# Optimization experiments

Hardware: AMD Instinct MI355X
Metric: run time of the kernel (lower is better)

Reference implementation:

```python
import jax, jax.numpy as jnp
import numpy as np

STEPS = 10      # raymarch_steps
HIDDEN = 16     # LSTM hidden size (hardcoded in module)
F_CH = 256      # num_feature_channels
B, N = 4, 8192  # batch, rays per batch element


def setup_inputs() -> dict:
    key = jax.random.key(0)
    ks = jax.random.split(key, 16)
    # rigid cam2world: random rotation (QR) + translation, bottom row [0,0,0,1]
    Q, _ = jnp.linalg.qr(jax.random.normal(ks[0], (B, 3, 3)))
    t = 0.5 * jax.random.normal(ks[1], (B, 3)) + jnp.array([0.0, 0.0, -2.5])
    cam2world = (jnp.zeros((B, 4, 4))
                 .at[:, :3, :3].set(Q)
                 .at[:, :3, 3].set(t)
                 .at[:, 3, 3].set(1.0))
    uv = jax.random.uniform(ks[2], (B, N, 2)) * 128.0  # pixel coords, 128x128 image
    intrinsics = jnp.tile(jnp.array([[128.0, 0.0, 64.0],
                                     [0.0, 128.0, 64.0],
                                     [0.0, 0.0, 1.0]]), (B, 1, 1))
    # torch forward draws N(0.05, 0.0005); lifted to an input for determinism
    initial_depth = 0.05 + 0.0005 * jax.random.normal(ks[3], (B, N, 1))
    g = lambda k, s, fan: jax.random.normal(k, s) * (1.0 / np.sqrt(fan))
    W1 = g(ks[4], (3, F_CH), 3); b1 = jnp.zeros((F_CH,))
    W2 = g(ks[5], (F_CH, F_CH), F_CH); b2 = jnp.zeros((F_CH,))
    W3 = g(ks[6], (F_CH, F_CH), F_CH); b3 = jnp.zeros((F_CH,))
    w_ih = g(ks[7], (4 * HIDDEN, F_CH), F_CH)
    w_hh = g(ks[8], (4 * HIDDEN, HIDDEN), HIDDEN)
    # forget-gate bias init = 1 (lstm_forget_gate_init fills [n//4:n//2] of each bias)
    fg = jnp.zeros((4 * HIDDEN,)).at[HIDDEN:2 * HIDDEN].set(1.0)
    b_ih = fg; b_hh = fg
    w_out = g(ks[9], (1, HIDDEN), HIDDEN); b_out = jnp.zeros((1,))
    return dict(cam2world=cam2world, uv=uv, intrinsics=intrinsics,
                initial_depth=initial_depth, W1=W1, b1=b1, W2=W2, b2=b2,
                W3=W3, b3=b3, w_ih=w_ih, w_hh=w_hh, b_ih=b_ih, b_hh=b_hh,
                w_out=w_out, b_out=b_out)


def world_from_xy_depth(xy, depth, intrinsics, cam2world):
    fx = intrinsics[:, 0:1, 0]; fy = intrinsics[:, 1:2, 1]
    cx = intrinsics[:, 0:1, 2]; cy = intrinsics[:, 1:2, 2]
    z = depth[..., 0]                                   # (B,N)
    x_lift = (xy[..., 0] - cx) / fx * z
    y_lift = (xy[..., 1] - cy) / fy * z
    pts_cam = jnp.stack([x_lift, y_lift, z, jnp.ones_like(z)], axis=-1)  # (B,N,4)
    return jnp.einsum('bij,bnj->bni', cam2world, pts_cam)[..., :3]


def get_ray_directions(xy, cam2world, intrinsics):
    z = jnp.ones(xy.shape[:2] + (1,), xy.dtype)
    pts = world_from_xy_depth(xy, z, intrinsics, cam2world)
    rd = pts - cam2world[:, None, :3, 3]
    return rd / jnp.linalg.norm(rd, axis=-1, keepdims=True)


def depth_from_world(world_coords, cam2world):
    hom = jnp.concatenate([world_coords, jnp.ones_like(world_coords[..., :1])], axis=-1)
    cam = jnp.einsum('bij,bnj->bni', jnp.linalg.inv(cam2world), hom)
    return cam[..., 2:3]


# identity in fwd, clamps grad to [-10,10] in bwd (matches register_hook in torch)
@jax.custom_vjp
def grad_clamp(x):
    return x

def _gc_fwd(x):
    return x, None

def _gc_bwd(_, g):
    return (jnp.clip(g, -10.0, 10.0),)

grad_clamp.defvjp(_gc_fwd, _gc_bwd)


def reference(cam2world, uv, intrinsics, initial_depth,
              W1, b1, W2, b2, W3, b3, w_ih, w_hh, b_ih, b_hh, w_out, b_out):
    B_, N_ = uv.shape[:2]
    ray_dirs = get_ray_directions(uv, cam2world, intrinsics)      # (B,N,3)
    wc0 = world_from_xy_depth(uv, initial_depth, intrinsics, cam2world)

    def phi(x):  # (B,N,3) -> (B,N,F_CH)
        h = jax.nn.relu(x @ W1 + b1)
        h = jax.nn.relu(h @ W2 + b2)
        return h @ W3 + b3

    def step(carry, _):
        wc, h, c = carry
        v = phi(wc).reshape(-1, F_CH)                             # (B*N, F)
        gates = v @ w_ih.T + b_ih + h @ w_hh.T + b_hh             # (B*N, 4H)
        i, f, g, o = jnp.split(gates, 4, axis=-1)
        c_new = jax.nn.sigmoid(f) * c + jax.nn.sigmoid(i) * jnp.tanh(g)
        h_new = grad_clamp(jax.nn.sigmoid(o) * jnp.tanh(c_new))
        sd = (h_new @ w_out.T + b_out).reshape(B_, N_, 1)         # signed distance
        return (wc + ray_dirs * sd, h_new, c_new), None

    h0 = jnp.zeros((B_ * N_, HIDDEN), uv.dtype)
    c0 = jnp.zeros((B_ * N_, HIDDEN), uv.dtype)
    (wc, _, _), _ = jax.lax.scan(step, (wc0, h0, c0), None, length=STEPS)
    return wc, depth_from_world(wc, cam2world)
```

## Files before the change

### kernel.cpp

```cpp
#include <hip/hip_runtime.h>
#include <hip/hip_bf16.h>


typedef __attribute__((ext_vector_type(8)))  __bf16 bf16x8;
typedef __attribute__((ext_vector_type(4)))  __bf16 bf16x4;
typedef __attribute__((ext_vector_type(4)))  float  f32x4;

#define H1S 264
#define H2S 296
#define GPAD 68

static __device__ __forceinline__ float sigmoidf_(float x) {
  return 1.0f / (1.0f + __expf(-x));
}
static __device__ __forceinline__ float tanhf_(float x) {
  return 1.0f - 2.0f / (__expf(2.0f * x) + 1.0f);
}
static __device__ __forceinline__ float ldin(const void* p, int i, bool f32) {
  return f32 ? ((const float*)p)[i] : (float)(((const __bf16*)p)[i]);
}
static __device__ __forceinline__ bool probe_f32(const void* intr) {
  return (*(const unsigned*)intr) == 0x43000000u;
}

__global__ void prep_kernel(const void* __restrict__ W2,
                            const void* __restrict__ W3,
                            const void* __restrict__ w_ih,
                            const void* __restrict__ b3,
                            const void* __restrict__ b_ih,
                            const void* __restrict__ b_hh,
                            const void* __restrict__ w_hh,
                            const void* __restrict__ intr,
                            __bf16* __restrict__ w2p,
                            __bf16* __restrict__ wfp,
                            float* __restrict__ bfv) {
  const bool f32 = probe_f32(intr);
  const int t = threadIdx.x;
  const int blk = blockIdx.x;
  __shared__ float stg[12480];

  if (blk < 256) {
    int idx = blk * 256 + t;
    int j = idx & 7, l = (idx >> 3) & 63, kt = (idx >> 9) & 7, nt = idx >> 12;
    int k = kt * 32 + ((l >> 4) << 3) + j;
    int n = nt * 16 + (l & 15);
    w2p[idx] = (__bf16)ldin(W2, k * 256 + n, f32);
  } else if (blk < 288) {
    int bb = blk - 256;
    int gt = bb >> 3, kt = bb & 7;
    float* wih_s = stg;
    float* w3_s = stg + 16 * 260;
    for (int i = t; i < 16 * 256; i += 256)
      wih_s[(i >> 8) * 260 + (i & 255)] =
          ldin(w_ih, (gt * 16 + (i >> 8)) * 256 + (i & 255), f32);
    for (int i = t; i < 32 * 256; i += 256)
      w3_s[(i >> 8) * 260 + (i & 255)] =
          ldin(W3, (kt * 32 + (i >> 8)) * 256 + (i & 255), f32);
    __syncthreads();
    #pragma unroll
    for (int h = 0; h < 2; ++h) {
      int o = t + h * 256;
      int l = o >> 3, j = o & 7;
      int kl = ((l >> 4) << 3) + j;
      int gl = l & 15;
      const f32x4* wa = (const f32x4*)&w3_s[kl * 260];
      const f32x4* wb = (const f32x4*)&wih_s[gl * 260];
      f32x4 acc = (f32x4){0.f, 0.f, 0.f, 0.f};
      #pragma unroll 8
      for (int m = 0; m < 64; ++m) acc += wa[m] * wb[m];
      wfp[((gt * 9 + kt) * 64 + l) * 8 + j] =
          (__bf16)(acc.x + acc.y + acc.z + acc.w);
    }
  } else if (blk == 288) {
    #pragma unroll
    for (int h = 0; h < 2; ++h) {
      int o = t + h * 256;
      int l = o >> 3, j = o & 7;
      int kl = ((l >> 4) << 3) + j;
      #pragma unroll
      for (int gt = 0; gt < 4; ++gt) {
        int g = gt * 16 + (l & 15);
        wfp[((gt * 9 + 8) * 64 + l) * 8 + j] =
            (__bf16)ldin(w_hh, g * 16 + (kl & 15), f32);
      }
    }
  } else {
    int g = t & 63, part = t >> 6;
    float acc = 0.f;
    for (int m = part * 64; m < part * 64 + 64; ++m)
      acc += ldin(b3, m, f32) * ldin(w_ih, g * 256 + m, f32);
    stg[t] = acc;
    __syncthreads();
    if (t < 64)
      bfv[t] = ldin(b_ih, t, f32) + ldin(b_hh, t, f32)
             + stg[t] + stg[64 + t] + stg[128 + t] + stg[192 + t];
  }
}

struct __align__(16) SMEM {
  union {
    __bf16 h1[64 * H1S];
    float  gates[64 * GPAD];
  } u;
  __bf16 h2[64 * H2S];
  float  wc_s[64][4];
  float  rd_s[64][4];
  float  b2s[256];
  float  cam_s[20];
  __bf16 W1s[768];
  __bf16 b1s[256];
};

__global__ __launch_bounds__(512, 4)
void ray_kernel(const void* __restrict__ cam2world,
                const void* __restrict__ uv,
                const void* __restrict__ intr,
                const void* __restrict__ d0,
                const void* __restrict__ W1,
                const void* __restrict__ b1,
                const void* __restrict__ b2,
                const void* __restrict__ w_out,
                const void* __restrict__ b_out,
                const __bf16* __restrict__ w2p,
                const __bf16* __restrict__ wfp,
                const float* __restrict__ bfv,
                void* __restrict__ out) {
  __shared__ SMEM sm;
  const bool f32 = probe_f32(intr);
  const int t = threadIdx.x;
  const int wg = blockIdx.x;
  const int b = wg >> 7;
  const int w = t >> 6;
  const int l = t & 63;
  const int q = l >> 4;
  const int m16 = l & 15;

  if (t == 0) {
    float A[9], T[3];
    for (int i = 0; i < 3; ++i) {
      for (int j2 = 0; j2 < 3; ++j2)
        A[i * 3 + j2] = ldin(cam2world, b * 16 + i * 4 + j2, f32);
      T[i] = ldin(cam2world, b * 16 + i * 4 + 3, f32);
    }
    float fx = ldin(intr, b * 9 + 0, f32), fy = ldin(intr, b * 9 + 4, f32);
    float cx = ldin(intr, b * 9 + 2, f32), cy = ldin(intr, b * 9 + 5, f32);
    float det = A[0] * (A[4] * A[8] - A[5] * A[7])
              - A[1] * (A[3] * A[8] - A[5] * A[6])
              + A[2] * (A[3] * A[7] - A[4] * A[6]);
    float gd = 1.0f / det;
    sm.cam_s[0] = fx; sm.cam_s[1] = fy; sm.cam_s[2] = cx; sm.cam_s[3] = cy;
    for (int i = 0; i < 9; ++i) sm.cam_s[4 + i] = A[i];
    for (int i = 0; i < 3; ++i) sm.cam_s[13 + i] = T[i];
    sm.cam_s[16] = (A[3] * A[7] - A[4] * A[6]) * gd;
    sm.cam_s[17] = (A[1] * A[6] - A[0] * A[7]) * gd;
    sm.cam_s[18] = (A[0] * A[4] - A[1] * A[3]) * gd;
    sm.cam_s[19] = 0.f;
  }
  for (int i = t; i < 768; i += 512) sm.W1s[i] = (__bf16)ldin(W1, i, f32);
  if (t < 256) {
    sm.b1s[t] = (__bf16)ldin(b1, t, f32);
    sm.b2s[t] = ldin(b2, t, f32);
  }
  for (int i = t; i < 1024; i += 512)
    *(unsigned*)&sm.h2[(i >> 4) * H2S + 256 + (i & 15) * 2] = 0u;
  __syncthreads();

  if (t < 64) {
    int R = wg * 64 + t;
    float fx = sm.cam_s[0], fy = sm.cam_s[1], cx = sm.cam_s[2], cy = sm.cam_s[3];
    const float* A = &sm.cam_s[4];
    const float* T = &sm.cam_s[13];
    float u = ldin(uv, 2 * R, f32), v = ldin(uv, 2 * R + 1, f32);
    float z = ldin(d0, R, f32);
    float xl = (u - cx) / fx, yl = (v - cy) / fy;
    float dx = A[0] * xl + A[1] * yl + A[2];
    float dy = A[3] * xl + A[4] * yl + A[5];
    float dz = A[6] * xl + A[7] * yl + A[8];
    float inv = 1.0f / sqrtf(dx * dx + dy * dy + dz * dz);
    sm.rd_s[t][0] = dx * inv; sm.rd_s[t][1] = dy * inv; sm.rd_s[t][2] = dz * inv;
    sm.rd_s[t][3] = 0.f;
    float xz = xl * z, yz = yl * z;
    sm.wc_s[t][0] = A[0] * xz + A[1] * yz + A[2] * z + T[0];
    sm.wc_s[t][1] = A[3] * xz + A[4] * yz + A[5] * z + T[1];
    sm.wc_s[t][2] = A[6] * xz + A[7] * yz + A[8] * z + T[2];
    sm.wc_s[t][3] = 0.f;
  }

  const bf16x8* w2f = (const bf16x8*)w2p;
  const bf16x8* wff = (const bf16x8*)wfp;
  const int gt = w >> 1;
  const int rtb = (w & 1) * 2;
  const float bf_i = bfv[m16], bf_f = bfv[16 + m16];
  const float bf_g = bfv[32 + m16], bf_o = bfv[48 + m16];
  const float wout_j = ldin(w_out, m16, f32);
  const float boutf = ldin(b_out, 0, f32);
  const int rA = t >> 4;
  float c_reg[2] = {0.f, 0.f};
  __syncthreads();

  for (int s = 0; s < 10; ++s) {
    {
      const int r = t >> 3;
      const int kb = (t & 7) * 32;
      f32x4 wcv = *(const f32x4*)&sm.wc_s[r][0];
      #pragma unroll
      for (int c2 = 0; c2 < 4; ++c2) {
        int k = kb + c2 * 8;
        bf16x8 a0 = *(const bf16x8*)&sm.W1s[k];
        bf16x8 a1 = *(const bf16x8*)&sm.W1s[256 + k];
        bf16x8 a2 = *(const bf16x8*)&sm.W1s[512 + k];
        bf16x8 bb = *(const bf16x8*)&sm.b1s[k];
        bf16x8 o;
        #pragma unroll
        for (int i = 0; i < 8; ++i) {
          float h = fmaf(wcv.x, (float)a0[i],
                    fmaf(wcv.y, (float)a1[i],
                    fmaf(wcv.z, (float)a2[i], (float)bb[i])));
          o[i] = (__bf16)fmaxf(h, 0.0f);
        }
        *(bf16x8*)&sm.u.h1[r * H1S + k] = o;
      }
    }
    __syncthreads();

    {
      #pragma unroll 1
      for (int ci = 0; ci < 2; ++ci) {
        const int ft = 2 * w + ci;
        f32x4 acc[4];
        #pragma unroll
        for (int rt = 0; rt < 4; ++rt) acc[rt] = (f32x4){0.f, 0.f, 0.f, 0.f};
        #pragma unroll
        for (int kt = 0; kt < 8; ++kt) {
          bf16x8 wa = w2f[(ft * 8 + kt) * 64 + l];
          #pragma unroll
          for (int rt = 0; rt < 4; ++rt) {
            bf16x8 hb = *(const bf16x8*)&sm.u.h1[(rt * 16 + m16) * H1S + kt * 32 + q * 8];
            acc[rt] = __builtin_amdgcn_mfma_f32_16x16x32_bf16(wa, hb, acc[rt], 0, 0, 0);
          }
        }
        f32x4 bias = *(const f32x4*)&sm.b2s[ft * 16 + q * 4];
        int f0 = ft * 16 + q * 4;
        #pragma unroll
        for (int rt = 0; rt < 4; ++rt) {
          int ray = rt * 16 + m16;
          bf16x4 pk;
          #pragma unroll
          for (int p = 0; p < 4; ++p)
            pk[p] = (__bf16)fmaxf(acc[rt][p] + bias[p], 0.0f);
          *(bf16x4*)&sm.h2[ray * H2S + f0] = pk;
        }
      }
    }
    __syncthreads();

    {
      f32x4 a3[2];
      a3[0] = (f32x4){0.f, 0.f, 0.f, 0.f};
      a3[1] = (f32x4){0.f, 0.f, 0.f, 0.f};
      #pragma unroll
      for (int kt = 0; kt < 9; ++kt) {
        bf16x8 wa = wff[(gt * 9 + kt) * 64 + l];
        #pragma unroll
        for (int u2 = 0; u2 < 2; ++u2) {
          bf16x8 hb = *(const bf16x8*)&sm.h2[((rtb + u2) * 16 + m16) * H2S + kt * 32 + q * 8];
          a3[u2] = __builtin_amdgcn_mfma_f32_16x16x32_bf16(wa, hb, a3[u2], 0, 0, 0);
        }
      }
      #pragma unroll
      for (int u2 = 0; u2 < 2; ++u2) {
        int ray = (rtb + u2) * 16 + m16;
        *(f32x4*)&sm.u.gates[ray * GPAD + gt * 16 + q * 4] = a3[u2];
      }
    }
    __syncthreads();

    {
      #pragma unroll
      for (int u2 = 0; u2 < 2; ++u2) {
        int rr = rA + u2 * 32;
        const float* gr = &sm.u.gates[rr * GPAD];
        float il = gr[m16] + bf_i;
        float fl = gr[16 + m16] + bf_f;
        float gl = gr[32 + m16] + bf_g;
        float ol = gr[48 + m16] + bf_o;
        float ii = sigmoidf_(il);
        float ff = sigmoidf_(fl);
        float gg = tanhf_(gl);
        float oo = sigmoidf_(ol);
        float cn = fmaf(ff, c_reg[u2], ii * gg);
        c_reg[u2] = cn;
        float hn = oo * tanhf_(cn);
        __bf16 hhi = (__bf16)hn;
        sm.h2[rr * H2S + 256 + m16] = hhi;
        sm.h2[rr * H2S + 272 + m16] = (__bf16)(hn - (float)hhi);
        float pv = hn * wout_j;
        pv += __shfl_xor(pv, 1);
        pv += __shfl_xor(pv, 2);
        pv += __shfl_xor(pv, 4);
        pv += __shfl_xor(pv, 8);
        if (m16 == 0) {
          float sd = pv + boutf;
          sm.wc_s[rr][0] = fmaf(sm.rd_s[rr][0], sd, sm.wc_s[rr][0]);
          sm.wc_s[rr][1] = fmaf(sm.rd_s[rr][1], sd, sm.wc_s[rr][1]);
          sm.wc_s[rr][2] = fmaf(sm.rd_s[rr][2], sd, sm.wc_s[rr][2]);
        }
      }
    }
    __syncthreads();
  }

  if (t < 64) {
    int R = wg * 64 + t;
    const float* T = &sm.cam_s[13];
    float x = sm.wc_s[t][0], y = sm.wc_s[t][1], z = sm.wc_s[t][2];
    float dep = sm.cam_s[16] * (x - T[0]) + sm.cam_s[17] * (y - T[1])
              + sm.cam_s[18] * (z - T[2]);
    if (f32) {
      float* o = (float*)out;
      o[R * 3 + 0] = x;
      o[R * 3 + 1] = y;
      o[R * 3 + 2] = z;
      o[98304 + R] = dep;
    } else {
      __bf16* o = (__bf16*)out;
      o[R * 3 + 0] = (__bf16)x;
      o[R * 3 + 1] = (__bf16)y;
      o[R * 3 + 2] = (__bf16)z;
      o[98304 + R] = (__bf16)dep;
    }
  }
}

extern "C" void kernel_launch(void* const* d_in, const int* in_sizes, int n_in,
                              void* d_out, int out_size, void* d_ws, size_t ws_size,
                              hipStream_t stream) {
  (void)in_sizes; (void)n_in; (void)out_size; (void)ws_size;
  const void* cam  = d_in[0];
  const void* uv   = d_in[1];
  const void* intr = d_in[2];
  const void* dep0 = d_in[3];
  const void* W1   = d_in[4];
  const void* b1   = d_in[5];
  const void* W2   = d_in[6];
  const void* b2   = d_in[7];
  const void* W3   = d_in[8];
  const void* b3   = d_in[9];
  const void* wih  = d_in[10];
  const void* whh  = d_in[11];
  const void* bih  = d_in[12];
  const void* bhh  = d_in[13];
  const void* wout = d_in[14];
  const void* bout = d_in[15];

  __bf16* w2p = (__bf16*)d_ws;
  __bf16* wfp = (__bf16*)((char*)d_ws + 131072);
  float*  bfv = (float*)((char*)d_ws + 167936);

  prep_kernel<<<290, 256, 0, stream>>>(W2, W3, wih, b3, bih, bhh, whh, intr,
                                       w2p, wfp, bfv);
  ray_kernel<<<512, 512, 0, stream>>>(cam, uv, intr, dep0, W1, b1, b2,
                                      wout, bout, w2p, wfp, bfv, d_out);
}
```

Measured before the change: 195.5 us.

## Move first layer onto MFMA and fuse LSTM gates into the gate matmul

Layer 1 (3→256) now runs on MFMA, using prepacked W1 with a split-bf16 input (hi/lo plus a bias column) in place of scalar FMAs. LSTM gate rows are permuted so each MFMA output lane holds i,f,g,o for one hidden unit. This lets the gate nonlinearity run directly on the accumulators, removing the gates shared-memory round trip and one barrier per step. Layer-2 work is split by ray tile with weights looped inside, the h state is double-buffered in h2, and the signed-distance reduction goes through partial sums applied at the start of the next step. The cost is more prep work, extra LDS (h1 no longer shares a union with gates) and a wider h2 stride, which may lower occupancy.

```diff
diff --git a/kernel.cpp b/kernel.cpp
--- a/kernel.cpp
+++ b/kernel.cpp
@@ -7,8 +7,7 @@
 typedef __attribute__((ext_vector_type(4)))  float  f32x4;
 
 #define H1S 264
-#define H2S 296
-#define GPAD 68
+#define H2S 328
 
 static __device__ __forceinline__ float sigmoidf_(float x) {
   return 1.0f / (1.0f + __expf(-x));
@@ -30,9 +29,12 @@
                             const void* __restrict__ b_ih,
                             const void* __restrict__ b_hh,
                             const void* __restrict__ w_hh,
+                            const void* __restrict__ W1,
+                            const void* __restrict__ b1,
                             const void* __restrict__ intr,
                             __bf16* __restrict__ w2p,
                             __bf16* __restrict__ wfp,
+                            __bf16* __restrict__ w1p,
                             float* __restrict__ bfv) {
   const bool f32 = probe_f32(intr);
   const int t = threadIdx.x;
@@ -50,9 +52,11 @@
     int gt = bb >> 3, kt = bb & 7;
     float* wih_s = stg;
     float* w3_s = stg + 16 * 260;
-    for (int i = t; i < 16 * 256; i += 256)
-      wih_s[(i >> 8) * 260 + (i & 255)] =
-          ldin(w_ih, (gt * 16 + (i >> 8)) * 256 + (i & 255), f32);
+    for (int i = t; i < 16 * 256; i += 256) {
+      int rl = i >> 8;
+      int g = (rl & 3) * 16 + gt * 4 + (rl >> 2);
+      wih_s[rl * 260 + (i & 255)] = ldin(w_ih, g * 256 + (i & 255), f32);
+    }
     for (int i = t; i < 32 * 256; i += 256)
       w3_s[(i >> 8) * 260 + (i & 255)] =
           ldin(W3, (kt * 32 + (i >> 8)) * 256 + (i & 255), f32);
@@ -79,12 +83,13 @@
       int kl = ((l >> 4) << 3) + j;
       #pragma unroll
       for (int gt = 0; gt < 4; ++gt) {
-        int g = gt * 16 + (l & 15);
+        int R = gt * 16 + (l & 15);
+        int g = (R & 3) * 16 + (R >> 2);
         wfp[((gt * 9 + 8) * 64 + l) * 8 + j] =
             (__bf16)ldin(w_hh, g * 16 + (kl & 15), f32);
       }
     }
-  } else {
+  } else if (blk == 289) {
     int g = t & 63, part = t >> 6;
     float acc = 0.f;
     for (int m = part * 64; m < part * 64 + 64; ++m)
@@ -94,21 +99,32 @@
     if (t < 64)
       bfv[t] = ldin(b_ih, t, f32) + ldin(b_hh, t, f32)
              + stg[t] + stg[64 + t] + stg[128 + t] + stg[192 + t];
+  } else {
+    for (int h = 0; h < 32; ++h) {
+      int o = h * 256 + t;
+      int ft = o >> 9, s2 = o & 511;
+      int l = s2 >> 3, j = s2 & 7;
+      int feat = ft * 16 + (l & 15);
+      int k = ((l >> 4) << 3) + j;
+      float v = 0.f;
+      if (k < 3) v = ldin(W1, k * 256 + feat, f32);
+      else if (k < 6) v = ldin(W1, (k - 3) * 256 + feat, f32);
+      else if (k == 6) v = ldin(b1, feat, f32);
+      w1p[o] = (__bf16)v;
+    }
   }
 }
 
 struct __align__(16) SMEM {
-  union {
-    __bf16 h1[64 * H1S];
-    float  gates[64 * GPAD];
-  } u;
+  __bf16 h1[64 * H1S];
   __bf16 h2[64 * H2S];
   float  wc_s[64][4];
   float  rd_s[64][4];
   float  b2s[256];
+  float  sd_part[4 * 64];
+  __bf16 wcf[512];
+  __bf16 zbuf[8];
   float  cam_s[20];
-  __bf16 W1s[768];
-  __bf16 b1s[256];
 };
 
 __global__ __launch_bounds__(512, 4)
@@ -116,13 +132,12 @@
                 const void* __restrict__ uv,
                 const void* __restrict__ intr,
                 const void* __restrict__ d0,
-                const void* __restrict__ W1,
-                const void* __restrict__ b1,
                 const void* __restrict__ b2,
                 const void* __restrict__ w_out,
                 const void* __restrict__ b_out,
                 const __bf16* __restrict__ w2p,
                 const __bf16* __restrict__ wfp,
+                const __bf16* __restrict__ w1p,
                 const float* __restrict__ bfv,
                 void* __restrict__ out) {
   __shared__ SMEM sm;
@@ -156,13 +171,10 @@
     sm.cam_s[18] = (A[0] * A[4] - A[1] * A[3]) * gd;
     sm.cam_s[19] = 0.f;
   }
-  for (int i = t; i < 768; i += 512) sm.W1s[i] = (__bf16)ldin(W1, i, f32);
-  if (t < 256) {
-    sm.b1s[t] = (__bf16)ldin(b1, t, f32);
-    sm.b2s[t] = ldin(b2, t, f32);
-  }
-  for (int i = t; i < 1024; i += 512)
-    *(unsigned*)&sm.h2[(i >> 4) * H2S + 256 + (i & 15) * 2] = 0u;
+  if (t < 256) sm.b2s[t] = ldin(b2, t, f32);
+  for (int i = t; i < 2048; i += 512)
+    *(unsigned*)&sm.h2[(i >> 5) * H2S + 256 + (i & 31) * 2] = 0u;
+  if (t < 4) *(unsigned*)&sm.zbuf[t * 2] = 0u;
   __syncthreads();
 
   if (t < 64) {
@@ -188,67 +200,93 @@
 
   const bf16x8* w2f = (const bf16x8*)w2p;
   const bf16x8* wff = (const bf16x8*)wfp;
-  const int gt = w >> 1;
-  const int rtb = (w & 1) * 2;
-  const float bf_i = bfv[m16], bf_f = bfv[16 + m16];
-  const float bf_g = bfv[32 + m16], bf_o = bfv[48 + m16];
-  const float wout_j = ldin(w_out, m16, f32);
+  const bf16x8* w1f = (const bf16x8*)w1p;
+  const int rt3 = w >> 1;
+  const int gtb = (w & 1) * 2;
+  float bfr[2][4], wout_h[2];
+  #pragma unroll
+  for (int k2 = 0; k2 < 2; ++k2) {
+    int hh = (gtb + k2) * 4 + q;
+    #pragma unroll
+    for (int p = 0; p < 4; ++p) bfr[k2][p] = bfv[p * 16 + hh];
+    wout_h[k2] = ldin(w_out, hh, f32);
+  }
   const float boutf = ldin(b_out, 0, f32);
-  const int rA = t >> 4;
   float c_reg[2] = {0.f, 0.f};
   __syncthreads();
 
   for (int s = 0; s < 10; ++s) {
+    if (t < 64) {
+      float wcx = sm.wc_s[t][0], wcy = sm.wc_s[t][1], wcz = sm.wc_s[t][2];
+      if (s > 0) {
+        float sd = sm.sd_part[t] + sm.sd_part[64 + t] + sm.sd_part[128 + t]
+                 + sm.sd_part[192 + t] + boutf;
+        wcx = fmaf(sm.rd_s[t][0], sd, wcx);
+        wcy = fmaf(sm.rd_s[t][1], sd, wcy);
+        wcz = fmaf(sm.rd_s[t][2], sd, wcz);
+        sm.wc_s[t][0] = wcx; sm.wc_s[t][1] = wcy; sm.wc_s[t][2] = wcz;
+      }
+      __bf16 hx = (__bf16)wcx, hy = (__bf16)wcy, hz = (__bf16)wcz;
+      bf16x8 pk;
+      pk[0] = hx; pk[1] = hy; pk[2] = hz;
+      pk[3] = (__bf16)(wcx - (float)hx);
+      pk[4] = (__bf16)(wcy - (float)hy);
+      pk[5] = (__bf16)(wcz - (float)hz);
+      pk[6] = (__bf16)1.0f; pk[7] = (__bf16)0.0f;
+      *(bf16x8*)&sm.wcf[t * 8] = pk;
+    }
+    __syncthreads();
+
     {
-      const int r = t >> 3;
-      const int kb = (t & 7) * 32;
-      f32x4 wcv = *(const f32x4*)&sm.wc_s[r][0];
+      bf16x8 wa0 = w1f[(2 * w) * 64 + l];
+      bf16x8 wa1 = w1f[(2 * w + 1) * 64 + l];
       #pragma unroll
-      for (int c2 = 0; c2 < 4; ++c2) {
-        int k = kb + c2 * 8;
-        bf16x8 a0 = *(const bf16x8*)&sm.W1s[k];
-        bf16x8 a1 = *(const bf16x8*)&sm.W1s[256 + k];
-        bf16x8 a2 = *(const bf16x8*)&sm.W1s[512 + k];
-        bf16x8 bb = *(const bf16x8*)&sm.b1s[k];
-        bf16x8 o;
-        #pragma unroll
-        for (int i = 0; i < 8; ++i) {
-          float h = fmaf(wcv.x, (float)a0[i],
-                    fmaf(wcv.y, (float)a1[i],
-                    fmaf(wcv.z, (float)a2[i], (float)bb[i])));
-          o[i] = (__bf16)fmaxf(h, 0.0f);
+      for (int rt = 0; rt < 4; ++rt) {
+        const __bf16* wsrc = (l < 16) ? &sm.wcf[(rt * 16 + l) * 8] : sm.zbuf;
+        bf16x8 hb = *(const bf16x8*)wsrc;
+        f32x4 a0 = __builtin_amdgcn_mfma_f32_16x16x32_bf16(
+            wa0, hb, (f32x4){0.f, 0.f, 0.f, 0.f}, 0, 0, 0);
+        f32x4 a1 = __builtin_amdgcn_mfma_f32_16x16x32_bf16(
+            wa1, hb, (f32x4){0.f, 0.f, 0.f, 0.f}, 0, 0, 0);
+        int ray = rt * 16 + m16;
+        bf16x4 o0, o1;
+        #pragma unroll
+        for (int p = 0; p < 4; ++p) {
+          o0[p] = (__bf16)fmaxf(a0[p], 0.0f);
+          o1[p] = (__bf16)fmaxf(a1[p], 0.0f);
         }
-        *(bf16x8*)&sm.u.h1[r * H1S + k] = o;
+        *(bf16x4*)&sm.h1[ray * H1S + (2 * w) * 16 + q * 4] = o0;
+        *(bf16x4*)&sm.h1[ray * H1S + (2 * w + 1) * 16 + q * 4] = o1;
       }
     }
     __syncthreads();
 
     {
+      const int rt2 = w >> 1;
+      const int fb = (w & 1) * 8;
       #pragma unroll 1
-      for (int ci = 0; ci < 2; ++ci) {
-        const int ft = 2 * w + ci;
+      for (int pass = 0; pass < 2; ++pass) {
         f32x4 acc[4];
         #pragma unroll
-        for (int rt = 0; rt < 4; ++rt) acc[rt] = (f32x4){0.f, 0.f, 0.f, 0.f};
+        for (int i = 0; i < 4; ++i) acc[i] = (f32x4){0.f, 0.f, 0.f, 0.f};
         #pragma unroll
         for (int kt = 0; kt < 8; ++kt) {
-          bf16x8 wa = w2f[(ft * 8 + kt) * 64 + l];
+          bf16x8 hb = *(const bf16x8*)&sm.h1[(rt2 * 16 + m16) * H1S + kt * 32 + q * 8];
           #pragma unroll
-          for (int rt = 0; rt < 4; ++rt) {
-            bf16x8 hb = *(const bf16x8*)&sm.u.h1[(rt * 16 + m16) * H1S + kt * 32 + q * 8];
-            acc[rt] = __builtin_amdgcn_mfma_f32_16x16x32_bf16(wa, hb, acc[rt], 0, 0, 0);
+          for (int i = 0; i < 4; ++i) {
+            bf16x8 wa = w2f[((fb + pass * 4 + i) * 8 + kt) * 64 + l];
+            acc[i] = __builtin_amdgcn_mfma_f32_16x16x32_bf16(wa, hb, acc[i], 0, 0, 0);
           }
         }
-        f32x4 bias = *(const f32x4*)&sm.b2s[ft * 16 + q * 4];
-        int f0 = ft * 16 + q * 4;
-        #pragma unroll
-        for (int rt = 0; rt < 4; ++rt) {
-          int ray = rt * 16 + m16;
+        #pragma unroll
+        for (int i = 0; i < 4; ++i) {
+          int ft = fb + pass * 4 + i;
+          f32x4 bias = *(const f32x4*)&sm.b2s[ft * 16 + q * 4];
           bf16x4 pk;
           #pragma unroll
           for (int p = 0; p < 4; ++p)
-            pk[p] = (__bf16)fmaxf(acc[rt][p] + bias[p], 0.0f);
-          *(bf16x4*)&sm.h2[ray * H2S + f0] = pk;
+            pk[p] = (__bf16)fmaxf(acc[i][p] + bias[p], 0.0f);
+          *(bf16x4*)&sm.h2[(rt2 * 16 + m16) * H2S + ft * 16 + q * 4] = pk;
         }
       }
     }
@@ -258,53 +296,36 @@
       f32x4 a3[2];
       a3[0] = (f32x4){0.f, 0.f, 0.f, 0.f};
       a3[1] = (f32x4){0.f, 0.f, 0.f, 0.f};
+      const int rb = (rt3 * 16 + m16) * H2S;
       #pragma unroll
       for (int kt = 0; kt < 9; ++kt) {
-        bf16x8 wa = wff[(gt * 9 + kt) * 64 + l];
-        #pragma unroll
-        for (int u2 = 0; u2 < 2; ++u2) {
-          bf16x8 hb = *(const bf16x8*)&sm.h2[((rtb + u2) * 16 + m16) * H2S + kt * 32 + q * 8];
-          a3[u2] = __builtin_amdgcn_mfma_f32_16x16x32_bf16(wa, hb, a3[u2], 0, 0, 0);
+        int koff = (kt == 8) ? (256 + (s & 1) * 32) : kt * 32;
+        bf16x8 hb = *(const bf16x8*)&sm.h2[rb + koff + q * 8];
+        #pragma unroll
+        for (int k2 = 0; k2 < 2; ++k2) {
+          bf16x8 wa = wff[((gtb + k2) * 9 + kt) * 64 + l];
+          a3[k2] = __builtin_amdgcn_mfma_f32_16x16x32_bf16(wa, hb, a3[k2], 0, 0, 0);
         }
       }
+      int ray = rt3 * 16 + m16;
+      int wb2 = 256 + ((s + 1) & 1) * 32;
       #pragma unroll
-      for (int u2 = 0; u2 < 2; ++u2) {
-        int ray = (rtb + u2) * 16 + m16;
-        *(f32x4*)&sm.u.gates[ray * GPAD + gt * 16 + q * 4] = a3[u2];
-      }
-    }
-    __syncthreads();
-
-    {
-      #pragma unroll
-      for (int u2 = 0; u2 < 2; ++u2) {
-        int rr = rA + u2 * 32;
-        const float* gr = &sm.u.gates[rr * GPAD];
-        float il = gr[m16] + bf_i;
-        float fl = gr[16 + m16] + bf_f;
-        float gl = gr[32 + m16] + bf_g;
-        float ol = gr[48 + m16] + bf_o;
-        float ii = sigmoidf_(il);
-        float ff = sigmoidf_(fl);
-        float gg = tanhf_(gl);
-        float oo = sigmoidf_(ol);
-        float cn = fmaf(ff, c_reg[u2], ii * gg);
-        c_reg[u2] = cn;
+      for (int k2 = 0; k2 < 2; ++k2) {
+        int hh = (gtb + k2) * 4 + q;
+        float ii = sigmoidf_(a3[k2][0] + bfr[k2][0]);
+        float ff = sigmoidf_(a3[k2][1] + bfr[k2][1]);
+        float gg = tanhf_(a3[k2][2] + bfr[k2][2]);
+        float oo = sigmoidf_(a3[k2][3] + bfr[k2][3]);
+        float cn = fmaf(ff, c_reg[k2], ii * gg);
+        c_reg[k2] = cn;
         float hn = oo * tanhf_(cn);
         __bf16 hhi = (__bf16)hn;
-        sm.h2[rr * H2S + 256 + m16] = hhi;
-        sm.h2[rr * H2S + 272 + m16] = (__bf16)(hn - (float)hhi);
-        float pv = hn * wout_j;
-        pv += __shfl_xor(pv, 1);
-        pv += __shfl_xor(pv, 2);
-        pv += __shfl_xor(pv, 4);
-        pv += __shfl_xor(pv, 8);
-        if (m16 == 0) {
-          float sd = pv + boutf;
-          sm.wc_s[rr][0] = fmaf(sm.rd_s[rr][0], sd, sm.wc_s[rr][0]);
-          sm.wc_s[rr][1] = fmaf(sm.rd_s[rr][1], sd, sm.wc_s[rr][1]);
-          sm.wc_s[rr][2] = fmaf(sm.rd_s[rr][2], sd, sm.wc_s[rr][2]);
-        }
+        sm.h2[ray * H2S + wb2 + hh] = hhi;
+        sm.h2[ray * H2S + wb2 + 16 + hh] = (__bf16)(hn - (float)hhi);
+        float pv = hn * wout_h[k2];
+        pv += __shfl_xor(pv, 16);
+        pv += __shfl_xor(pv, 32);
+        if (l < 16) sm.sd_part[(gtb + k2) * 64 + ray] = pv;
       }
     }
     __syncthreads();
@@ -313,7 +334,11 @@
   if (t < 64) {
     int R = wg * 64 + t;
     const float* T = &sm.cam_s[13];
-    float x = sm.wc_s[t][0], y = sm.wc_s[t][1], z = sm.wc_s[t][2];
+    float sd = sm.sd_part[t] + sm.sd_part[64 + t] + sm.sd_part[128 + t]
+             + sm.sd_part[192 + t] + boutf;
+    float x = fmaf(sm.rd_s[t][0], sd, sm.wc_s[t][0]);
+    float y = fmaf(sm.rd_s[t][1], sd, sm.wc_s[t][1]);
+    float z = fmaf(sm.rd_s[t][2], sd, sm.wc_s[t][2]);
     float dep = sm.cam_s[16] * (x - T[0]) + sm.cam_s[17] * (y - T[1])
               + sm.cam_s[18] * (z - T[2]);
     if (f32) {
@@ -355,10 +380,11 @@
 
   __bf16* w2p = (__bf16*)d_ws;
   __bf16* wfp = (__bf16*)((char*)d_ws + 131072);
-  float*  bfv = (float*)((char*)d_ws + 167936);
-
-  prep_kernel<<<290, 256, 0, stream>>>(W2, W3, wih, b3, bih, bhh, whh, intr,
-                                       w2p, wfp, bfv);
-  ray_kernel<<<512, 512, 0, stream>>>(cam, uv, intr, dep0, W1, b1, b2,
-                                      wout, bout, w2p, wfp, bfv, d_out);
-}
+  __bf16* w1p = (__bf16*)((char*)d_ws + 167936);
+  float*  bfv = (float*)((char*)d_ws + 184320);
+
+  prep_kernel<<<291, 256, 0, stream>>>(W2, W3, wih, b3, bih, bhh, whh,
+                                       W1, b1, intr, w2p, wfp, w1p, bfv);
+  ray_kernel<<<512, 512, 0, stream>>>(cam, uv, intr, dep0, b2,
+                                      wout, bout, w2p, wfp, w1p, bfv, d_out);
+}
```

Result: slower. 300.7 us (+53.8%).
